# Performance work log

Hardware: AMD Instinct MI355X
Metric: run time of the kernel (lower is better)

Reference implementation:

```python
import jax, jax.numpy as jnp
import numpy as np

# Natural-order 4x4 Hadamard matrix (H @ H = 4*I); 2D inverse WHT scale = 1/16.
H4 = np.array([[1, 1, 1, 1],
               [1, -1, 1, -1],
               [1, 1, -1, -1],
               [1, -1, -1, 1]], dtype=np.float32)

B, NH, NW, C, K = 16, 28, 28, 64, 64  # out_channels=192 -> K=64 per branch


def setup_inputs() -> dict:
    key = jax.random.key(0)
    ks = jax.random.split(key, 9)
    d = {}
    for i, n in enumerate(['transIm1', 'transIm2', 'transIm3']):
        d[n] = jax.random.normal(ks[i], (16, B, NH, NW, C), dtype=jnp.float32)
    for i, n in enumerate(['weight1', 'weight2', 'weight3']):
        d[n] = jax.random.normal(ks[3 + i], (16, C, K), dtype=jnp.float32) * 0.05
    for i, n in enumerate(['bias1', 'bias2', 'bias3']):
        d[n] = jax.random.normal(ks[6 + i], (1, 1, 1, K), dtype=jnp.float32) * 0.05
    return d


def _iwht_branch(trans, w, b):
    # Per-WHT-coefficient channel matmul: [16,B,nH,nW,C] x [16,C,K] -> [16,B,nH,nW,K]
    y = jnp.einsum('tbijc,tck->tbijk', trans, w)
    _, Bb, nH, nW, Kk = y.shape
    y = y.reshape(4, 4, Bb, nH, nW, Kk)  # coeff index t = 4*u + v
    h = jnp.asarray(H4, y.dtype)
    # Inverse 2D WHT per 4x4 block, scatter blocks back to pixel grid.
    z = jnp.einsum('pu,qv,uvbijk->bipjqk', h, h, y) * (1.0 / 16.0)
    return z.reshape(Bb, 4 * nH, 4 * nW, Kk) + b


def reference(transIm1, transIm2, transIm3, weight1, weight2, weight3,
              bias1, bias2, bias3):
    out1 = _iwht_branch(transIm1, weight1, bias1)
    out2 = _iwht_branch(transIm2, weight2, bias2)
    out3 = _iwht_branch(transIm3, weight3, bias3)
    return (out1, out2, out3)
```

## Files before the change

kernel.cpp:

```cpp
#include <hip/hip_runtime.h>
#include <hip/hip_bf16.h>


typedef __attribute__((ext_vector_type(8))) short bf16x8;
typedef __attribute__((ext_vector_type(4))) float floatx4;

#define NSITES 12544
#define NTILES 784
#define OUT_PER_BRANCH 12845056
#define WT_ELEMS (3*16*64*64)
#define ROW_F 68
#define CHUNK_F (64 * ROW_F)

__device__ __forceinline__ short f32_to_bf16_bits(float f) {
    __hip_bfloat16 h = __float2bfloat16(f);
    return *reinterpret_cast<short*>(&h);
}

__global__ void transpose_weights(const float* __restrict__ w0,
                                  const float* __restrict__ w1,
                                  const float* __restrict__ w2,
                                  __hip_bfloat16* __restrict__ wT) {
    int idx = blockIdx.x * blockDim.x + threadIdx.x;
    if (idx >= WT_ELEMS) return;
    int c  = idx & 63;
    int k  = (idx >> 6) & 63;
    int t  = (idx >> 12) & 15;
    int br = idx >> 16;
    const float* w = (br == 0) ? w0 : ((br == 1) ? w1 : w2);
    wT[idx] = __float2bfloat16(w[(t * 64 + c) * 64 + k]);
}

template <bool USE_WT>
__global__ __launch_bounds__(256, 4) void iwht_kernel(
    const float* __restrict__ x0, const float* __restrict__ x1,
    const float* __restrict__ x2,
    const float* __restrict__ w0, const float* __restrict__ w1,
    const float* __restrict__ w2,
    const __hip_bfloat16* __restrict__ wT,
    const float* __restrict__ b0, const float* __restrict__ b1,
    const float* __restrict__ b2,
    float* __restrict__ out) {
    __shared__ float xs[2][CHUNK_F];

    int bx   = blockIdx.x;
    int br   = bx / NTILES;
    int tile = bx - br * NTILES;
    int lane = threadIdx.x & 63;
    int wave = threadIdx.x >> 6;
    int l15  = lane & 15;
    int quad = lane >> 4;
    int n    = wave * 16 + l15;

    const float* x    = (br == 0) ? x0 : ((br == 1) ? x1 : x2);
    const float* w    = (br == 0) ? w0 : ((br == 1) ? w1 : w2);
    const float* bias = (br == 0) ? b0 : ((br == 1) ? b1 : b2);

    const float* xg = x + (size_t)(tile * 16) * 64 + lane;

    floatx4 acc[16];
#pragma unroll
    for (int t = 0; t < 16; t++) acc[t] = (floatx4){0.f, 0.f, 0.f, 0.f};

#define STAGE(g, buf)                                                          \
    {                                                                          \
        _Pragma("unroll") for (int r = 0; r < 16; r++) {                       \
            int row = wave * 16 + r;                      \
            int tl  = row >> 4;                                                \
            int s   = row & 15;                                                \
            const float* gp = xg + ((size_t)((g) * 4 + tl) * NSITES + s) * 64; \
            __builtin_amdgcn_global_load_lds(                                  \
                (const __attribute__((address_space(1))) void*)gp,             \
                (__attribute__((address_space(3))) void*)&xs[buf][row * ROW_F],\
                4, 0, 0);                                                      \
        }                                                                      \
    }

    STAGE(0, 0);
    __syncthreads();

#pragma unroll
    for (int g = 0; g < 4; g++) {
        int buf = g & 1;
        if (g < 3) STAGE(g + 1, buf ^ 1);
#pragma unroll
        for (int tl = 0; tl < 4; tl++) {
            int t = g * 4 + tl;
            const float* rowp = &xs[buf][(tl * 16 + l15) * ROW_F + quad * 8];
            floatx4 f0 = ((const floatx4*)rowp)[0];
            floatx4 f1 = ((const floatx4*)rowp)[1];
            floatx4 f2 = ((const floatx4*)(rowp + 32))[0];
            floatx4 f3 = ((const floatx4*)(rowp + 32))[1];
            bf16x8 a0, a1;
#pragma unroll
            for (int j = 0; j < 4; j++) {
                a0[j]     = f32_to_bf16_bits(f0[j]);
                a0[j + 4] = f32_to_bf16_bits(f1[j]);
                a1[j]     = f32_to_bf16_bits(f2[j]);
                a1[j + 4] = f32_to_bf16_bits(f3[j]);
            }
            bf16x8 bb0, bb1;
            if (USE_WT) {
                const bf16x8* wv = reinterpret_cast<const bf16x8*>(
                    wT + (((size_t)(br * 16 + t) * 64 + n) * 64) + quad * 8);
                bb0 = wv[0];
                bb1 = wv[4];
            } else {
#pragma unroll
                for (int j = 0; j < 8; j++) {
                    int c0 = quad * 8 + j;
                    bb0[j] = f32_to_bf16_bits(w[(t * 64 + c0) * 64 + n]);
                    bb1[j] = f32_to_bf16_bits(w[(t * 64 + c0 + 32) * 64 + n]);
                }
            }
            acc[t] = __builtin_amdgcn_mfma_f32_16x16x32_bf16(bb0, a0, acc[t], 0, 0, 0);
            acc[t] = __builtin_amdgcn_mfma_f32_16x16x32_bf16(bb1, a1, acc[t], 0, 0, 0);
        }
        if (g < 3) __syncthreads();
    }
#undef STAGE

    int k0   = wave * 16 + quad * 4;
    int site = tile * 16 + l15;
    int b    = site / 784;
    int rem  = site - b * 784;
    int i    = rem / 28;
    int j    = rem - i * 28;
    float* op = out + (size_t)br * OUT_PER_BRANCH +
                (((size_t)(b * 112 + 4 * i)) * 112 + 4 * j) * 64 + k0;
    floatx4 bias4 = *reinterpret_cast<const floatx4*>(bias + k0);

#pragma unroll
    for (int u = 0; u < 4; u++) {
        floatx4 y0 = acc[4 * u + 0], y1 = acc[4 * u + 1];
        floatx4 y2 = acc[4 * u + 2], y3 = acc[4 * u + 3];
        floatx4 A = y0 + y2, Bv = y1 + y3, Cv = y0 - y2, Dv = y1 - y3;
        acc[4 * u + 0] = A + Bv;
        acc[4 * u + 1] = A - Bv;
        acc[4 * u + 2] = Cv + Dv;
        acc[4 * u + 3] = Cv - Dv;
    }

#pragma unroll
    for (int q = 0; q < 4; q++) {
        floatx4 z0 = acc[0 + q], z1 = acc[4 + q], z2 = acc[8 + q], z3 = acc[12 + q];
        floatx4 A = z0 + z2, Bv = z1 + z3, Cv = z0 - z2, Dv = z1 - z3;
        floatx4 o[4];
        o[0] = A + Bv;
        o[1] = A - Bv;
        o[2] = Cv + Dv;
        o[3] = Cv - Dv;
#pragma unroll
        for (int p = 0; p < 4; p++) {
            floatx4 v = o[p] * 0.0625f + bias4;
            *reinterpret_cast<floatx4*>(op + (size_t)(p * 112 + q) * 64) = v;
        }
    }
}

extern "C" void kernel_launch(void* const* d_in, const int* in_sizes, int n_in,
                              void* d_out, int out_size, void* d_ws, size_t ws_size,
                              hipStream_t stream) {
    const float* x0 = (const float*)d_in[0];
    const float* x1 = (const float*)d_in[1];
    const float* x2 = (const float*)d_in[2];
    const float* w0 = (const float*)d_in[3];
    const float* w1 = (const float*)d_in[4];
    const float* w2 = (const float*)d_in[5];
    const float* b0 = (const float*)d_in[6];
    const float* b1 = (const float*)d_in[7];
    const float* b2 = (const float*)d_in[8];
    float* out = (float*)d_out;
    __hip_bfloat16* wT = (__hip_bfloat16*)d_ws;

    bool use_wt = ws_size >= (size_t)WT_ELEMS * sizeof(__hip_bfloat16);
    if (use_wt) {
        transpose_weights<<<(WT_ELEMS + 255) / 256, 256, 0, stream>>>(w0, w1, w2, wT);
        iwht_kernel<true><<<3 * NTILES, 256, 0, stream>>>(x0, x1, x2, w0, w1, w2, wT,
                                                          b0, b1, b2, out);
    } else {
        iwht_kernel<false><<<3 * NTILES, 256, 0, stream>>>(x0, x1, x2, w0, w1, w2, wT,
                                                           b0, b1, b2, out);
    }
}
```

Baseline: 302.8 us.

## Load activations directly from global into registers, dropping LDS staging

Removes the double-buffered LDS staging of the input tile via global_load_lds and the block barriers. Each wave now reads its activation fragments straight from global memory with vector loads. All four waves load the same 16x64 activation rows, so the inputs are fetched four times, relying on L2/L1 to absorb the duplication. The occupancy hint is lowered from 4 to 3 blocks per CU to give more registers for the in-flight loads.

New measurement: 339.6 us. 12.2% more time.

```diff
diff --git a/kernel.cpp b/kernel.cpp
--- a/kernel.cpp
+++ b/kernel.cpp
@@ -9,8 +9,6 @@
 #define NTILES 784
 #define OUT_PER_BRANCH 12845056
 #define WT_ELEMS (3*16*64*64)
-#define ROW_F 68
-#define CHUNK_F (64 * ROW_F)
 
 __device__ __forceinline__ short f32_to_bf16_bits(float f) {
     __hip_bfloat16 h = __float2bfloat16(f);
@@ -32,7 +30,7 @@
 }
 
 template <bool USE_WT>
-__global__ __launch_bounds__(256, 4) void iwht_kernel(
+__global__ __launch_bounds__(256, 3) void iwht_kernel(
     const float* __restrict__ x0, const float* __restrict__ x1,
     const float* __restrict__ x2,
     const float* __restrict__ w0, const float* __restrict__ w1,
@@ -41,8 +39,6 @@
     const float* __restrict__ b0, const float* __restrict__ b1,
     const float* __restrict__ b2,
     float* __restrict__ out) {
-    __shared__ float xs[2][CHUNK_F];
-
     int bx   = blockIdx.x;
     int br   = bx / NTILES;
     int tile = bx - br * NTILES;
@@ -56,69 +52,44 @@
     const float* w    = (br == 0) ? w0 : ((br == 1) ? w1 : w2);
     const float* bias = (br == 0) ? b0 : ((br == 1) ? b1 : b2);
 
-    const float* xg = x + (size_t)(tile * 16) * 64 + lane;
+    const float* xb = x + ((size_t)(tile * 16 + l15)) * 64 + quad * 8;
 
     floatx4 acc[16];
 #pragma unroll
     for (int t = 0; t < 16; t++) acc[t] = (floatx4){0.f, 0.f, 0.f, 0.f};
 
-#define STAGE(g, buf)                                                          \
-    {                                                                          \
-        _Pragma("unroll") for (int r = 0; r < 16; r++) {                       \
-            int row = wave * 16 + r;                      \
-            int tl  = row >> 4;                                                \
-            int s   = row & 15;                                                \
-            const float* gp = xg + ((size_t)((g) * 4 + tl) * NSITES + s) * 64; \
-            __builtin_amdgcn_global_load_lds(                                  \
-                (const __attribute__((address_space(1))) void*)gp,             \
-                (__attribute__((address_space(3))) void*)&xs[buf][row * ROW_F],\
-                4, 0, 0);                                                      \
-        }                                                                      \
+#pragma unroll
+    for (int t = 0; t < 16; t++) {
+        const float* xr = xb + (size_t)t * (NSITES * 64);
+        floatx4 f0 = ((const floatx4*)xr)[0];
+        floatx4 f1 = ((const floatx4*)xr)[1];
+        floatx4 f2 = ((const floatx4*)(xr + 32))[0];
+        floatx4 f3 = ((const floatx4*)(xr + 32))[1];
+        bf16x8 a0, a1;
+#pragma unroll
+        for (int j = 0; j < 4; j++) {
+            a0[j]     = f32_to_bf16_bits(f0[j]);
+            a0[j + 4] = f32_to_bf16_bits(f1[j]);
+            a1[j]     = f32_to_bf16_bits(f2[j]);
+            a1[j + 4] = f32_to_bf16_bits(f3[j]);
+        }
+        bf16x8 bb0, bb1;
+        if (USE_WT) {
+            const bf16x8* wv = reinterpret_cast<const bf16x8*>(
+                wT + (((size_t)(br * 16 + t) * 64 + n) * 64) + quad * 8);
+            bb0 = wv[0];
+            bb1 = wv[4];
+        } else {
+#pragma unroll
+            for (int j = 0; j < 8; j++) {
+                int c0 = quad * 8 + j;
+                bb0[j] = f32_to_bf16_bits(w[(t * 64 + c0) * 64 + n]);
+                bb1[j] = f32_to_bf16_bits(w[(t * 64 + c0 + 32) * 64 + n]);
+            }
+        }
+        acc[t] = __builtin_amdgcn_mfma_f32_16x16x32_bf16(bb0, a0, acc[t], 0, 0, 0);
+        acc[t] = __builtin_amdgcn_mfma_f32_16x16x32_bf16(bb1, a1, acc[t], 0, 0, 0);
     }
-
-    STAGE(0, 0);
-    __syncthreads();
-
-#pragma unroll
-    for (int g = 0; g < 4; g++) {
-        int buf = g & 1;
-        if (g < 3) STAGE(g + 1, buf ^ 1);
-#pragma unroll
-        for (int tl = 0; tl < 4; tl++) {
-            int t = g * 4 + tl;
-            const float* rowp = &xs[buf][(tl * 16 + l15) * ROW_F + quad * 8];
-            floatx4 f0 = ((const floatx4*)rowp)[0];
-            floatx4 f1 = ((const floatx4*)rowp)[1];
-            floatx4 f2 = ((const floatx4*)(rowp + 32))[0];
-            floatx4 f3 = ((const floatx4*)(rowp + 32))[1];
-            bf16x8 a0, a1;
-#pragma unroll
-            for (int j = 0; j < 4; j++) {
-                a0[j]     = f32_to_bf16_bits(f0[j]);
-                a0[j + 4] = f32_to_bf16_bits(f1[j]);
-                a1[j]     = f32_to_bf16_bits(f2[j]);
-                a1[j + 4] = f32_to_bf16_bits(f3[j]);
-            }
-            bf16x8 bb0, bb1;
-            if (USE_WT) {
-                const bf16x8* wv = reinterpret_cast<const bf16x8*>(
-                    wT + (((size_t)(br * 16 + t) * 64 + n) * 64) + quad * 8);
-                bb0 = wv[0];
-                bb1 = wv[4];
-            } else {
-#pragma unroll
-                for (int j = 0; j < 8; j++) {
-                    int c0 = quad * 8 + j;
-                    bb0[j] = f32_to_bf16_bits(w[(t * 64 + c0) * 64 + n]);
-                    bb1[j] = f32_to_bf16_bits(w[(t * 64 + c0 + 32) * 64 + n]);
-                }
-            }
-            acc[t] = __builtin_amdgcn_mfma_f32_16x16x32_bf16(bb0, a0, acc[t], 0, 0, 0);
-            acc[t] = __builtin_amdgcn_mfma_f32_16x16x32_bf16(bb1, a1, acc[t], 0, 0, 0);
-        }
-        if (g < 3) __syncthreads();
-    }
-#undef STAGE
 
     int k0   = wave * 16 + quad * 4;
     int site = tile * 16 + l15;
```

## Triple-buffer LDS staging with explicit vmcnt waits to deepen load pipeline

Applied to the files above, without the earlier changes.

Moves from a double-buffered LDS loop to a three-buffer schedule. Three chunks are issued up front and each compute stage waits with explicit s_waitcnt vmcnt counts plus barriers instead of full __syncthreads. This keeps more global loads in flight to hide memory latency. In exchange, the extra LDS buffer and the lower launch-bounds occupancy hint (4 to 3 blocks) reduce concurrent blocks per CU, and the hand-counted vmcnt values could be wrong if the weight global loads also count against vmcnt.

Result: no change. 298.3 us (-1.5%).

```diff
diff --git a/kernel.cpp b/kernel.cpp
--- a/kernel.cpp
+++ b/kernel.cpp
@@ -32,7 +32,7 @@
 }
 
 template <bool USE_WT>
-__global__ __launch_bounds__(256, 4) void iwht_kernel(
+__global__ __launch_bounds__(256, 3) void iwht_kernel(
     const float* __restrict__ x0, const float* __restrict__ x1,
     const float* __restrict__ x2,
     const float* __restrict__ w0, const float* __restrict__ w1,
@@ -41,7 +41,7 @@
     const float* __restrict__ b0, const float* __restrict__ b1,
     const float* __restrict__ b2,
     float* __restrict__ out) {
-    __shared__ float xs[2][CHUNK_F];
+    __shared__ float xs[3][CHUNK_F];
 
     int bx   = blockIdx.x;
     int br   = bx / NTILES;
@@ -76,49 +76,68 @@
         }                                                                      \
     }
 
+#define COMPUTE(g, buf)                                                        \
+    {                                                                          \
+        _Pragma("unroll") for (int tl = 0; tl < 4; tl++) {                     \
+            int t = (g) * 4 + tl;                                              \
+            const float* rowp = &xs[buf][(tl * 16 + l15) * ROW_F + quad * 8];  \
+            floatx4 f0 = ((const floatx4*)rowp)[0];                            \
+            floatx4 f1 = ((const floatx4*)rowp)[1];                            \
+            floatx4 f2 = ((const floatx4*)(rowp + 32))[0];                     \
+            floatx4 f3 = ((const floatx4*)(rowp + 32))[1];                     \
+            bf16x8 a0, a1;                                                     \
+            _Pragma("unroll") for (int j = 0; j < 4; j++) {                    \
+                a0[j]     = f32_to_bf16_bits(f0[j]);                           \
+                a0[j + 4] = f32_to_bf16_bits(f1[j]);                           \
+                a1[j]     = f32_to_bf16_bits(f2[j]);                           \
+                a1[j + 4] = f32_to_bf16_bits(f3[j]);                           \
+            }                                                                  \
+            bf16x8 bb0, bb1;                                                   \
+            if (USE_WT) {                                                      \
+                const bf16x8* wv = reinterpret_cast<const bf16x8*>(            \
+                    wT + (((size_t)(br * 16 + t) * 64 + n) * 64) + quad * 8);  \
+                bb0 = wv[0];                                                   \
+                bb1 = wv[4];                                                   \
+            } else {                                                           \
+                _Pragma("unroll") for (int j = 0; j < 8; j++) {                \
+                    int c0 = quad * 8 + j;                                     \
+                    bb0[j] = f32_to_bf16_bits(w[(t * 64 + c0) * 64 + n]);      \
+                    bb1[j] = f32_to_bf16_bits(w[(t * 64 + c0 + 32) * 64 + n]); \
+                }                                                              \
+            }                                                                  \
+            acc[t] = __builtin_amdgcn_mfma_f32_16x16x32_bf16(bb0, a0, acc[t],  \
+                                                             0, 0, 0);         \
+            acc[t] = __builtin_amdgcn_mfma_f32_16x16x32_bf16(bb1, a1, acc[t],  \
+                                                             0, 0, 0);         \
+        }                                                                      \
+    }
+
+#define WAITV(N)                                                               \
+    asm volatile("s_waitcnt vmcnt(" #N ")" ::: "memory");                      \
+    __builtin_amdgcn_s_barrier();                                              \
+    __builtin_amdgcn_sched_barrier(0);
+
     STAGE(0, 0);
-    __syncthreads();
-
-#pragma unroll
-    for (int g = 0; g < 4; g++) {
-        int buf = g & 1;
-        if (g < 3) STAGE(g + 1, buf ^ 1);
-#pragma unroll
-        for (int tl = 0; tl < 4; tl++) {
-            int t = g * 4 + tl;
-            const float* rowp = &xs[buf][(tl * 16 + l15) * ROW_F + quad * 8];
-            floatx4 f0 = ((const floatx4*)rowp)[0];
-            floatx4 f1 = ((const floatx4*)rowp)[1];
-            floatx4 f2 = ((const floatx4*)(rowp + 32))[0];
-            floatx4 f3 = ((const floatx4*)(rowp + 32))[1];
-            bf16x8 a0, a1;
-#pragma unroll
-            for (int j = 0; j < 4; j++) {
-                a0[j]     = f32_to_bf16_bits(f0[j]);
-                a0[j + 4] = f32_to_bf16_bits(f1[j]);
-                a1[j]     = f32_to_bf16_bits(f2[j]);
-                a1[j + 4] = f32_to_bf16_bits(f3[j]);
-            }
-            bf16x8 bb0, bb1;
-            if (USE_WT) {
-                const bf16x8* wv = reinterpret_cast<const bf16x8*>(
-                    wT + (((size_t)(br * 16 + t) * 64 + n) * 64) + quad * 8);
-                bb0 = wv[0];
-                bb1 = wv[4];
-            } else {
-#pragma unroll
-                for (int j = 0; j < 8; j++) {
-                    int c0 = quad * 8 + j;
-                    bb0[j] = f32_to_bf16_bits(w[(t * 64 + c0) * 64 + n]);
-                    bb1[j] = f32_to_bf16_bits(w[(t * 64 + c0 + 32) * 64 + n]);
-                }
-            }
-            acc[t] = __builtin_amdgcn_mfma_f32_16x16x32_bf16(bb0, a0, acc[t], 0, 0, 0);
-            acc[t] = __builtin_amdgcn_mfma_f32_16x16x32_bf16(bb1, a1, acc[t], 0, 0, 0);
-        }
-        if (g < 3) __syncthreads();
-    }
+    STAGE(1, 1);
+    STAGE(2, 2);
+
+    WAITV(32);
+    COMPUTE(0, 0);
+    __builtin_amdgcn_s_barrier();
+    STAGE(3, 0);
+
+    WAITV(32);
+    COMPUTE(1, 1);
+
+    WAITV(16);
+    COMPUTE(2, 2);
+
+    WAITV(0);
+    COMPUTE(3, 0);
+
 #undef STAGE
+#undef COMPUTE
+#undef WAITV
 
     int k0   = wave * 16 + quad * 4;
     int site = tile * 16 + l15;
```
